# Performance work log

Measured on AMD Instinct MI355X. Metric: run time of the kernel, lower is better.

The kernel has to match this reference:

```python
import jax, jax.numpy as jnp
import numpy as np

B, S, ENC2, DEC = 32, 4096, 1024, 512

def setup_inputs() -> dict:
    key = jax.random.key(0)
    k1, k2, k3 = jax.random.split(key, 3)
    hidden = jax.random.normal(k1, (B, DEC), dtype=jnp.float32)
    context = jax.random.normal(k2, (B, S, ENC2), dtype=jnp.float32)
    mask = jnp.ones((B, S), dtype=jnp.int32)
    # Linear(enc*2+dec -> dec): weight [DEC, ENC2+DEC], bias [DEC]
    W_attn = jax.random.normal(k3, (DEC, ENC2 + DEC), dtype=jnp.float32) * (1.0 / np.sqrt(ENC2 + DEC))
    b_attn = jnp.zeros((DEC,), dtype=jnp.float32)
    v = jax.random.uniform(jax.random.fold_in(key, 7), (DEC,), dtype=jnp.float32)
    return {"hidden": hidden, "context": context, "mask": mask,
            "W_attn": W_attn, "b_attn": b_attn, "v": v}

def reference(hidden, context, mask, W_attn, b_attn, v):
    # cat((hidden repeated over S, context)) @ W.T == hidden@Wh.T + context@Wc.T
    # split W to avoid materializing the [B,S,1536] concat
    Wh = W_attn[:, :DEC]          # acts on hidden (first in cat)
    Wc = W_attn[:, DEC:]          # acts on context
    h_proj = hidden @ Wh.T + b_attn                      # [B, DEC]
    c_proj = jnp.einsum('bse,de->bsd', context, Wc)      # [B, S, DEC]
    sim = jnp.tanh(h_proj[:, None, :] + c_proj)          # [B, S, DEC]
    scores = jnp.einsum('bsd,d->bs', sim, v)             # [B, S]
    scores = jnp.where(mask == 0, -jnp.inf, scores)
    return jax.nn.softmax(scores, axis=1)
```

## Files before the change

kernel.cpp:

```cpp
#include <hip/hip_runtime.h>
#include <hip/hip_bf16.h>
#include <cmath>

#define NB 32
#define NS 4096
#define NK 1024
#define ND 512
#define WSTRIDE 1536
#define NT 32

using bf16x8 = __attribute__((ext_vector_type(8))) __bf16;
using f32x4  = __attribute__((ext_vector_type(4))) float;
typedef unsigned short u16;

__device__ inline u16 f2b(float x) {
    __hip_bfloat16 h = __float2bfloat16(x);
    u16 u; __builtin_memcpy(&u, &h, 2); return u;
}

__device__ inline float fast_tanh(float x) {
    float xc = fminf(fmaxf(x, -10.f), 10.f);
    float e = __expf(2.f * xc);
    return (e - 1.f) / (e + 1.f);
}

__global__ void pack_wc_kernel(const float* __restrict__ W, u16* __restrict__ wcb) {
    int idx = blockIdx.x * 256 + threadIdx.x;
    int R = idx >> 10, k = idx & 1023;
    float val = W[(size_t)R * WSTRIDE + ND + k];
    int ks = k >> 5, S = (k >> 3) & 3, j = k & 7;
    int g = (R << 2) + (S ^ ((R >> 1) & 3));
    wcb[(ks << 14) + (g << 3) + j] = f2b(val);
}

__global__ void hproj_kernel(const float* __restrict__ hidden, const float* __restrict__ W,
                             const float* __restrict__ bias, float* __restrict__ hp) {
    int b = blockIdx.x, d = threadIdx.x;
    __shared__ float sh[ND];
    sh[d] = hidden[b * ND + d];
    __syncthreads();
    const float4* wr = (const float4*)(W + (size_t)d * WSTRIDE);
    float acc = bias[d];
#pragma unroll 8
    for (int k = 0; k < ND / 4; k++) {
        float4 w4 = wr[k];
        acc += w4.x * sh[4 * k] + w4.y * sh[4 * k + 1] + w4.z * sh[4 * k + 2] + w4.w * sh[4 * k + 3];
    }
    hp[b * ND + d] = acc;
}

__global__ __launch_bounds__(1024, 4)
void fused_scores_kernel(const float* __restrict__ ctx, const u16* __restrict__ wcb,
                         const float* __restrict__ hp, const float* __restrict__ vvec,
                         float* __restrict__ scores) {
    __shared__ __align__(16) char lA[2][128 * 64];
    __shared__ __align__(16) char lB[2][512 * 64];

    const int tid = threadIdx.x;
    const int blk = blockIdx.x;
    const int b  = blk >> 5;
    const int s0 = (blk & 31) << 7;

    const int lane = tid & 63, wid = tid >> 6;
    const int l15 = lane & 15, l4 = lane >> 4;
    const int wm = wid >> 3, wn = wid & 7;

    const int srow = tid >> 3, q = tid & 7;
    const float4* asrc = (const float4*)(ctx + (size_t)b * NS * NK + (size_t)(s0 + srow) * NK);
    const int awbyte = (srow << 6) + ((((q >> 1) ^ ((srow >> 1) & 3))) << 4) + ((q & 1) << 3);

    int aoff[4], boff[4];
#pragma unroll
    for (int r = 0; r < 4; r++) {
        int row = (wm << 6) + (r << 4) + l15;
        aoff[r] = (row << 6) + ((l4 ^ ((row >> 1) & 3)) << 4);
    }
#pragma unroll
    for (int c = 0; c < 4; c++) {
        int row = (wn << 6) + (c << 4) + l15;
        boff[c] = (row << 6) + ((l4 ^ ((row >> 1) & 3)) << 4);
    }

    f32x4 acc[4][4];
    f32x4 zero = {0.f, 0.f, 0.f, 0.f};
#pragma unroll
    for (int r = 0; r < 4; r++)
#pragma unroll
        for (int c = 0; c < 4; c++) acc[r][c] = zero;

    const char* wcb_bytes = (const char*)wcb;
    float4 va;

#define STAGE_B_DMA(chunk, buf)                                                      \
    _Pragma("unroll")                                                                \
    for (int i = 0; i < 2; i++) {                                                    \
        const char* src = wcb_bytes + ((size_t)(chunk) << 15)                        \
                          + (((((wid << 1) + i) << 6) + lane) << 4);                 \
        __builtin_amdgcn_global_load_lds(                                            \
            (const __attribute__((address_space(1))) void*)src,                      \
            (__attribute__((address_space(3))) void*)(&lB[buf][((wid << 1) + i) << 10]), \
            16, 0, 0);                                                               \
    }

#define CVT_WRITE_A(buf)                                                             \
    {                                                                                \
        ushort4 a4;                                                                  \
        a4.x = f2b(va.x); a4.y = f2b(va.y); a4.z = f2b(va.z); a4.w = f2b(va.w);      \
        *(ushort4*)(&lA[buf][awbyte]) = a4;                                          \
    }

#define MFMA_CLUSTER(abuf, bbuf)                                                     \
    {                                                                                \
        bf16x8 af[4], bfr[4];                                                        \
        _Pragma("unroll")                                                            \
        for (int r = 0; r < 4; r++) af[r] = *(const bf16x8*)(&lA[abuf][aoff[r]]);    \
        _Pragma("unroll")                                                            \
        for (int c = 0; c < 4; c++) bfr[c] = *(const bf16x8*)(&lB[bbuf][boff[c]]);   \
        __builtin_amdgcn_s_setprio(1);                                               \
        _Pragma("unroll")                                                            \
        for (int r = 0; r < 4; r++)                                                  \
            _Pragma("unroll")                                                        \
            for (int c = 0; c < 4; c++)                                              \
                acc[r][c] = __builtin_amdgcn_mfma_f32_16x16x32_bf16(                 \
                    af[r], bfr[c], acc[r][c], 0, 0, 0);                              \
        __builtin_amdgcn_s_setprio(0);                                               \
    }

    STAGE_B_DMA(0, 0);
    va = asrc[q];
    asm volatile("s_waitcnt vmcnt(0)" ::: "memory");
    CVT_WRITE_A(0);
    va = asrc[8 + q];
    asm volatile("s_waitcnt lgkmcnt(0)" ::: "memory");
    __builtin_amdgcn_s_barrier();
    __builtin_amdgcn_sched_barrier(0);

#pragma unroll 2
    for (int t = 0; t < NT; t++) {
        const int cur = t & 1, nxt = cur ^ 1;
        const int cB = (t + 1 < NT) ? t + 1 : NT - 1;
        const int tA = (t + 2 < NT) ? t + 2 : NT - 1;

        STAGE_B_DMA(cB, nxt);
        asm volatile("s_waitcnt vmcnt(2)" ::: "memory");
        CVT_WRITE_A(nxt);
        va = asrc[(tA << 3) + q];
        MFMA_CLUSTER(cur, cur);
        asm volatile("s_waitcnt vmcnt(1) lgkmcnt(0)" ::: "memory");
        __builtin_amdgcn_s_barrier();
        __builtin_amdgcn_sched_barrier(0);
    }

    const float* hpb = hp + b * ND;
    float part[4][4];
#pragma unroll
    for (int r = 0; r < 4; r++)
#pragma unroll
        for (int i = 0; i < 4; i++) part[r][i] = 0.f;

#pragma unroll
    for (int c = 0; c < 4; c++) {
        int d = (wn << 6) + (c << 4) + l15;
        float hpv = hpb[d], vv = vvec[d];
#pragma unroll
        for (int r = 0; r < 4; r++)
#pragma unroll
            for (int i = 0; i < 4; i++)
                part[r][i] += fast_tanh(acc[r][c][i] + hpv) * vv;
    }

    float* sc = (float*)lA;
#pragma unroll
    for (int r = 0; r < 4; r++) {
#pragma unroll
        for (int i = 0; i < 4; i++) {
            float p = part[r][i];
            p += __shfl_xor(p, 1); p += __shfl_xor(p, 2);
            p += __shfl_xor(p, 4); p += __shfl_xor(p, 8);
            if (l15 == 0) sc[(wn << 7) + (wm << 6) + (r << 4) + (l4 << 2) + i] = p;
        }
    }
    __syncthreads();
    if (tid < 128) {
        float s = 0.f;
#pragma unroll
        for (int w = 0; w < 8; w++) s += sc[(w << 7) + tid];
        scores[(size_t)b * NS + s0 + tid] = s;
    }
}

__global__ void softmax_kernel(const float* __restrict__ scores, const int* __restrict__ mask,
                               float* __restrict__ out) {
    int b = blockIdx.x, tid = threadIdx.x;
    __shared__ float red[256];
    float loc[16];
    float mx = -INFINITY;
#pragma unroll
    for (int i = 0; i < 16; i++) {
        int idx = i * 256 + tid;
        float s = scores[b * NS + idx];
        if (mask[b * NS + idx] == 0) s = -INFINITY;
        loc[i] = s;
        mx = fmaxf(mx, s);
    }
    red[tid] = mx; __syncthreads();
    for (int off = 128; off; off >>= 1) { if (tid < off) red[tid] = fmaxf(red[tid], red[tid + off]); __syncthreads(); }
    mx = red[0]; __syncthreads();
    float sum = 0.f;
#pragma unroll
    for (int i = 0; i < 16; i++) { float e = __expf(loc[i] - mx); loc[i] = e; sum += e; }
    red[tid] = sum; __syncthreads();
    for (int off = 128; off; off >>= 1) { if (tid < off) red[tid] += red[tid + off]; __syncthreads(); }
    float inv = 1.f / red[0];
#pragma unroll
    for (int i = 0; i < 16; i++) out[b * NS + i * 256 + tid] = loc[i] * inv;
}

extern "C" void kernel_launch(void* const* d_in, const int* in_sizes, int n_in,
                              void* d_out, int out_size, void* d_ws, size_t ws_size,
                              hipStream_t stream) {
    const float* hidden  = (const float*)d_in[0];
    const float* context = (const float*)d_in[1];
    const int*   mask    = (const int*)d_in[2];
    const float* W_attn  = (const float*)d_in[3];
    const float* b_attn  = (const float*)d_in[4];
    const float* v       = (const float*)d_in[5];
    float* out           = (float*)d_out;

    char* ws = (char*)d_ws;
    u16*   wcb    = (u16*)ws;
    float* hp     = (float*)(ws + (1 << 20));
    float* scores = (float*)(ws + (1 << 20) + (64 << 10));

    pack_wc_kernel<<<2048, 256, 0, stream>>>(W_attn, wcb);
    hproj_kernel<<<NB, ND, 0, stream>>>(hidden, W_attn, b_attn, hp);
    fused_scores_kernel<<<NB * 32, 1024, 0, stream>>>(context, wcb, hp, v, scores);
    softmax_kernel<<<NB, 256, 0, stream>>>(scores, mask, out);
}
```

Measured before the change: 269.2 us.

## Load packed weight fragments directly from global and double the A k-tile

The packed Wc layout now stores each MFMA B fragment contiguously, so every wave reads its B operands straight from global/L2 into registers instead of DMA-staging a 512x32 tile through LDS. The context tile in LDS grows to a 64-wide k step with an 8-chunk XOR swizzle, which halves the outer iterations and barriers. Each iteration runs two MFMA clusters. This removes LDS traffic and the capacity used for B, but the kernel now waits on global latency for B inside the loop. The vmcnt(0) before the second cluster also forces the prefetched context loads to complete early, which can expose HBM latency.

```diff
diff --git a/kernel.cpp b/kernel.cpp
--- a/kernel.cpp
+++ b/kernel.cpp
@@ -7,9 +7,10 @@
 #define NK 1024
 #define ND 512
 #define WSTRIDE 1536
-#define NT 32
+#define NTO 16
 
 using bf16x8 = __attribute__((ext_vector_type(8))) __bf16;
+using u16x8  = __attribute__((ext_vector_type(8))) unsigned short;
 using f32x4  = __attribute__((ext_vector_type(4))) float;
 typedef unsigned short u16;
 
@@ -26,11 +27,12 @@
 
 __global__ void pack_wc_kernel(const float* __restrict__ W, u16* __restrict__ wcb) {
     int idx = blockIdx.x * 256 + threadIdx.x;
-    int R = idx >> 10, k = idx & 1023;
-    float val = W[(size_t)R * WSTRIDE + ND + k];
-    int ks = k >> 5, S = (k >> 3) & 3, j = k & 7;
-    int g = (R << 2) + (S ^ ((R >> 1) & 3));
-    wcb[(ks << 14) + (g << 3) + j] = f2b(val);
+    int d = idx >> 10, k = idx & 1023;
+    float val = W[(size_t)d * WSTRIDE + ND + k];
+    int ks = k >> 5, kk = (k >> 3) & 3, j = k & 7;
+    int n6 = d >> 6, c = (d >> 4) & 3, rr = d & 15;
+    int frag = (((ks << 3) + n6) << 2) + c;
+    wcb[frag * 512 + ((kk << 4) + rr) * 8 + j] = f2b(val);
 }
 
 __global__ void hproj_kernel(const float* __restrict__ hidden, const float* __restrict__ W,
@@ -53,8 +55,7 @@
 void fused_scores_kernel(const float* __restrict__ ctx, const u16* __restrict__ wcb,
                          const float* __restrict__ hp, const float* __restrict__ vvec,
                          float* __restrict__ scores) {
-    __shared__ __align__(16) char lA[2][128 * 64];
-    __shared__ __align__(16) char lB[2][512 * 64];
+    __shared__ __align__(16) char lA[2][128 * 128];
 
     const int tid = threadIdx.x;
     const int blk = blockIdx.x;
@@ -67,19 +68,16 @@
 
     const int srow = tid >> 3, q = tid & 7;
     const float4* asrc = (const float4*)(ctx + (size_t)b * NS * NK + (size_t)(s0 + srow) * NK);
-    const int awbyte = (srow << 6) + ((((q >> 1) ^ ((srow >> 1) & 3))) << 4) + ((q & 1) << 3);
-
-    int aoff[4], boff[4];
+    const int awbyte = (srow << 7) + ((q ^ (srow & 7)) << 4);
+
+    int aoff[4];
 #pragma unroll
     for (int r = 0; r < 4; r++) {
         int row = (wm << 6) + (r << 4) + l15;
-        aoff[r] = (row << 6) + ((l4 ^ ((row >> 1) & 3)) << 4);
-    }
-#pragma unroll
-    for (int c = 0; c < 4; c++) {
-        int row = (wn << 6) + (c << 4) + l15;
-        boff[c] = (row << 6) + ((l4 ^ ((row >> 1) & 3)) << 4);
-    }
+        aoff[r] = (row << 7) + ((l4 ^ (row & 7)) << 4);
+    }
+
+    const char* bptr = (const char*)wcb + (wn << 12) + (lane << 4);
 
     f32x4 acc[4][4];
     f32x4 zero = {0.f, 0.f, 0.f, 0.f};
@@ -88,65 +86,66 @@
 #pragma unroll
         for (int c = 0; c < 4; c++) acc[r][c] = zero;
 
-    const char* wcb_bytes = (const char*)wcb;
-    float4 va;
-
-#define STAGE_B_DMA(chunk, buf)                                                      \
-    _Pragma("unroll")                                                                \
-    for (int i = 0; i < 2; i++) {                                                    \
-        const char* src = wcb_bytes + ((size_t)(chunk) << 15)                        \
-                          + (((((wid << 1) + i) << 6) + lane) << 4);                 \
-        __builtin_amdgcn_global_load_lds(                                            \
-            (const __attribute__((address_space(1))) void*)src,                      \
-            (__attribute__((address_space(3))) void*)(&lB[buf][((wid << 1) + i) << 10]), \
-            16, 0, 0);                                                               \
-    }
+    float4 va0, va1;
 
 #define CVT_WRITE_A(buf)                                                             \
     {                                                                                \
-        ushort4 a4;                                                                  \
-        a4.x = f2b(va.x); a4.y = f2b(va.y); a4.z = f2b(va.z); a4.w = f2b(va.w);      \
-        *(ushort4*)(&lA[buf][awbyte]) = a4;                                          \
-    }
-
-#define MFMA_CLUSTER(abuf, bbuf)                                                     \
+        u16x8 a8;                                                                    \
+        a8[0] = f2b(va0.x); a8[1] = f2b(va0.y); a8[2] = f2b(va0.z); a8[3] = f2b(va0.w); \
+        a8[4] = f2b(va1.x); a8[5] = f2b(va1.y); a8[6] = f2b(va1.z); a8[7] = f2b(va1.w); \
+        *(u16x8*)(&lA[buf][awbyte]) = a8;                                            \
+    }
+
+#define MFMA16(afv, bfv)                                                             \
     {                                                                                \
-        bf16x8 af[4], bfr[4];                                                        \
-        _Pragma("unroll")                                                            \
-        for (int r = 0; r < 4; r++) af[r] = *(const bf16x8*)(&lA[abuf][aoff[r]]);    \
-        _Pragma("unroll")                                                            \
-        for (int c = 0; c < 4; c++) bfr[c] = *(const bf16x8*)(&lB[bbuf][boff[c]]);   \
         __builtin_amdgcn_s_setprio(1);                                               \
         _Pragma("unroll")                                                            \
         for (int r = 0; r < 4; r++)                                                  \
             _Pragma("unroll")                                                        \
             for (int c = 0; c < 4; c++)                                              \
                 acc[r][c] = __builtin_amdgcn_mfma_f32_16x16x32_bf16(                 \
-                    af[r], bfr[c], acc[r][c], 0, 0, 0);                              \
+                    afv[r], bfv[c], acc[r][c], 0, 0, 0);                             \
         __builtin_amdgcn_s_setprio(0);                                               \
     }
 
-    STAGE_B_DMA(0, 0);
-    va = asrc[q];
+    va0 = asrc[2 * q];
+    va1 = asrc[2 * q + 1];
     asm volatile("s_waitcnt vmcnt(0)" ::: "memory");
     CVT_WRITE_A(0);
-    va = asrc[8 + q];
+    va0 = asrc[16 + 2 * q];
+    va1 = asrc[16 + 2 * q + 1];
     asm volatile("s_waitcnt lgkmcnt(0)" ::: "memory");
     __builtin_amdgcn_s_barrier();
     __builtin_amdgcn_sched_barrier(0);
 
 #pragma unroll 2
-    for (int t = 0; t < NT; t++) {
-        const int cur = t & 1, nxt = cur ^ 1;
-        const int cB = (t + 1 < NT) ? t + 1 : NT - 1;
-        const int tA = (t + 2 < NT) ? t + 2 : NT - 1;
-
-        STAGE_B_DMA(cB, nxt);
-        asm volatile("s_waitcnt vmcnt(2)" ::: "memory");
+    for (int T = 0; T < NTO; T++) {
+        const int cur = T & 1, nxt = cur ^ 1;
+        const int tA = (T + 2 < NTO) ? T + 2 : NTO - 1;
+
+        bf16x8 af[4], bfr[4];
+
+#pragma unroll
+        for (int c = 0; c < 4; c++)
+            bfr[c] = *(const bf16x8*)(bptr + (T << 16) + (c << 10));
+#pragma unroll
+        for (int r = 0; r < 4; r++)
+            af[r] = *(const bf16x8*)(&lA[cur][aoff[r]]);
+        asm volatile("s_waitcnt vmcnt(4)" ::: "memory");
         CVT_WRITE_A(nxt);
-        va = asrc[(tA << 3) + q];
-        MFMA_CLUSTER(cur, cur);
-        asm volatile("s_waitcnt vmcnt(1) lgkmcnt(0)" ::: "memory");
+        va0 = asrc[tA * 16 + 2 * q];
+        va1 = asrc[tA * 16 + 2 * q + 1];
+        asm volatile("s_waitcnt vmcnt(2) lgkmcnt(0)" ::: "memory");
+        MFMA16(af, bfr);
+
+#pragma unroll
+        for (int c = 0; c < 4; c++)
+            bfr[c] = *(const bf16x8*)(bptr + (T << 16) + 32768 + (c << 10));
+#pragma unroll
+        for (int r = 0; r < 4; r++)
+            af[r] = *(const bf16x8*)(&lA[cur][aoff[r] ^ 64]);
+        asm volatile("s_waitcnt vmcnt(0) lgkmcnt(0)" ::: "memory");
+        MFMA16(af, bfr);
         __builtin_amdgcn_s_barrier();
         __builtin_amdgcn_sched_barrier(0);
     }
```

Measured after the change: 283.0 us. 5.1% more time.
